# Kernel optimization log

Hardware: AMD Instinct MI355X
Metric: run time of the kernel (lower is better)

The kernel has to match this reference:

```python
import jax, jax.numpy as jnp
import numpy as np

D_MODEL = 1024
NUM_HEADS = 16
HEAD_DIM = D_MODEL // NUM_HEADS
SEQ_LEN = 4096
BATCH = 1
ROPE_THETA = 10000.0


def apply_rope(x, theta):
    # x: [B, H, S, D], interleaved pair rotation (x_{2i}, x_{2i+1})
    D = x.shape[-1]
    S = x.shape[-2]
    pos = jnp.arange(S, dtype=jnp.float32)
    inv_freq = theta ** (-jnp.arange(0, D, 2, dtype=jnp.float32) / D)  # [D/2]
    ang = pos[:, None] * inv_freq[None, :]  # [S, D/2]
    cos = jnp.cos(ang).astype(x.dtype)
    sin = jnp.sin(ang).astype(x.dtype)
    x1 = x[..., 0::2]
    x2 = x[..., 1::2]
    r1 = x1 * cos - x2 * sin
    r2 = x1 * sin + x2 * cos
    return jnp.stack([r1, r2], axis=-1).reshape(x.shape)


def setup_inputs() -> dict:
    key = jax.random.key(0)
    ks = jax.random.split(key, 5)
    s = 1.0 / np.sqrt(D_MODEL)
    return {
        "x": jax.random.normal(ks[0], (BATCH, SEQ_LEN, D_MODEL), jnp.float32),
        "Wq": jax.random.normal(ks[1], (D_MODEL, D_MODEL), jnp.float32) * s,
        "Wk": jax.random.normal(ks[2], (D_MODEL, D_MODEL), jnp.float32) * s,
        "Wv": jax.random.normal(ks[3], (D_MODEL, D_MODEL), jnp.float32) * s,
        "Wo": jax.random.normal(ks[4], (D_MODEL, D_MODEL), jnp.float32) * s,
    }


def reference(x, Wq, Wk, Wv, Wo):
    B, S, _ = x.shape
    # bias-free linear: y = x @ W.T
    def proj(W):
        y = jnp.einsum('bsd,ed->bse', x, W)
        return y.reshape(B, S, NUM_HEADS, HEAD_DIM).transpose(0, 2, 1, 3)  # [B,H,S,hd]
    q = apply_rope(proj(Wq), ROPE_THETA)
    k = apply_rope(proj(Wk), ROPE_THETA)
    v = proj(Wv)
    scale = 1.0 / jnp.sqrt(jnp.asarray(HEAD_DIM, dtype=x.dtype))
    scores = jnp.einsum('bhqd,bhkd->bhqk', q, k) * scale  # [B,H,S,S]
    causal = jnp.tril(jnp.ones((S, S), dtype=bool))
    scores = jnp.where(causal, scores, jnp.asarray(-jnp.inf, dtype=scores.dtype))
    attn = jax.nn.softmax(scores, axis=-1)
    out = jnp.einsum('bhqk,bhkd->bhqd', attn, v)
    out = out.transpose(0, 2, 1, 3).reshape(B, S, D_MODEL)
    return jnp.einsum('bsd,ed->bse', out, Wo)
```

## Files before the change

### kernel.cpp

```cpp
#include <hip/hip_runtime.h>
#include <math.h>

#define SEQ 4096
#define DM  1024
#define NH  16

typedef __attribute__((ext_vector_type(8))) short bf16x8;
typedef __attribute__((ext_vector_type(4))) float f32x4;
typedef __attribute__((ext_vector_type(16))) float f32x16;
typedef __attribute__((ext_vector_type(4))) unsigned int u32x4;

#define QSCALE 0.18033688011112042f
#define SMAX 16.0f

__device__ __forceinline__ unsigned short f2bf(float f){
  unsigned int u = __float_as_uint(f);
  u += 0x7fffu + ((u >> 16) & 1u);
  return (unsigned short)(u >> 16);
}

__device__ __forceinline__ unsigned int cvtpk(float lo, float hi){
  unsigned int r;
  asm("v_cvt_pk_bf16_f32 %0, %1, %2" : "=v"(r) : "v"(lo), "v"(hi));
  return r;
}

__device__ __forceinline__ void gload_lds16(const void* g, void* l){
  __builtin_amdgcn_global_load_lds(
      (const __attribute__((address_space(1))) unsigned int*)g,
      (__attribute__((address_space(3))) unsigned int*)l,
      16, 0, 0);
}

__global__ __launch_bounds__(256) void prep_kernel(const float* __restrict__ x,
                                                   const float* __restrict__ Wq, const float* __restrict__ Wk,
                                                   const float* __restrict__ Wv, const float* __restrict__ Wo,
                                                   unsigned short* __restrict__ xb,
                                                   unsigned short* __restrict__ wqb, unsigned short* __restrict__ wkb,
                                                   unsigned short* __restrict__ wvb, unsigned short* __restrict__ wob,
                                                   float2* __restrict__ ropetab){
  const int sel = blockIdx.y;
  if (sel < 5){
    const float* src = (sel == 0) ? x : (sel == 1) ? Wq : (sel == 2) ? Wk : (sel == 3) ? Wv : Wo;
    unsigned short* dst = (sel == 0) ? xb : (sel == 1) ? wqb : (sel == 2) ? wkb : (sel == 3) ? wvb : wob;
    const int n4 = (sel == 0) ? SEQ * DM / 4 : DM * DM / 4;
    int i = blockIdx.x * 256 + threadIdx.x;
    int stride = gridDim.x * 256;
    for (; i < n4; i += stride){
      float4 v = ((const float4*)src)[i];
      ushort4 o; o.x = f2bf(v.x); o.y = f2bf(v.y); o.z = f2bf(v.z); o.w = f2bf(v.w);
      ((ushort4*)dst)[i] = o;
    }
  } else {
    int i = blockIdx.x * 256 + threadIdx.x;
    int stride = gridDim.x * 256;
    for (; i < SEQ * 32; i += stride){
      int s = i >> 5, f = i & 31;
      double inv = exp2(-(double)f * (13.287712379549449 / 32.0));
      double a = (double)s * inv;
      const double twopi = 6.283185307179586476;
      a -= twopi * floor(a / twopi);
      float af = (float)a;
      ropetab[i] = make_float2(cosf(af), sinf(af));
    }
  }
}

__global__ __launch_bounds__(256) void qkv_gemm(const unsigned short* __restrict__ A,
                                                const unsigned short* __restrict__ Wq,
                                                const unsigned short* __restrict__ Wk,
                                                const unsigned short* __restrict__ Wv,
                                                unsigned short* __restrict__ Qo,
                                                unsigned short* __restrict__ Ko,
                                                unsigned short* __restrict__ Vto,
                                                const float2* __restrict__ rope)
{
  __shared__ unsigned short At[128 * 64];
  __shared__ unsigned short Bt[128 * 64];
  const int sel = blockIdx.x >> 3;
  const unsigned short* B = (sel == 0) ? Wq : (sel == 1) ? Wk : Wv;
  const int K = DM;
  const int t = threadIdx.x;
  const int lane = t & 63, w = t >> 6;
  const int lg = lane >> 4, lr = lane & 15;
  const int wr = w >> 1, wc = w & 1;
  const int m0 = blockIdx.y * 128, n0 = (blockIdx.x & 7) * 128;

  f32x4 acc[4][4];
  #pragma unroll
  for (int mi = 0; mi < 4; mi++)
    #pragma unroll
    for (int nj = 0; nj < 4; nj++)
      acc[mi][nj] = (f32x4){0.f, 0.f, 0.f, 0.f};

  for (int k0 = 0; k0 < K; k0 += 64){
    __syncthreads();
    #pragma unroll
    for (int r = 0; r < 4; r++){
      int idx = r * 256 + t, row = idx >> 3, ch = idx & 7, cs = ch ^ (row & 7);
      gload_lds16(&A[(size_t)(m0 + row) * K + k0 + cs * 8], &At[idx * 8]);
    }
    #pragma unroll
    for (int r = 0; r < 4; r++){
      int idx = r * 256 + t, row = idx >> 3, ch = idx & 7, cs = ch ^ (row & 7);
      gload_lds16(&B[(size_t)(n0 + row) * K + k0 + cs * 8], &Bt[idx * 8]);
    }
    __syncthreads();
    #pragma unroll
    for (int kk = 0; kk < 2; kk++){
      bf16x8 af[4], bfr[4];
      #pragma unroll
      for (int mi = 0; mi < 4; mi++){
        int row = wr * 64 + mi * 16 + lr;
        af[mi] = *(const bf16x8*)&At[row * 64 + (((kk * 4 + lg) ^ (row & 7)) << 3)];
      }
      #pragma unroll
      for (int nj = 0; nj < 4; nj++){
        int row = wc * 64 + nj * 16 + lr;
        bfr[nj] = *(const bf16x8*)&Bt[row * 64 + (((kk * 4 + lg) ^ (row & 7)) << 3)];
      }
      #pragma unroll
      for (int mi = 0; mi < 4; mi++)
        #pragma unroll
        for (int nj = 0; nj < 4; nj++)
          acc[mi][nj] = __builtin_amdgcn_mfma_f32_16x16x32_bf16(af[mi], bfr[nj], acc[mi][nj], 0, 0, 0);
    }
  }

  #pragma unroll
  for (int mi = 0; mi < 4; mi++){
    #pragma unroll
    for (int nj = 0; nj < 4; nj++){
      f32x4 v = acc[mi][nj];
      int col  = n0 + wc * 64 + nj * 16 + lr;
      int row0 = m0 + wr * 64 + mi * 16 + lg * 4;
      if (sel == 0){
        #pragma unroll
        for (int j = 0; j < 4; j++){
          float val = v[j];
          float oth = __shfl_xor(val, 1);
          int row = row0 + j;
          int i = (col & 63) >> 1;
          float2 cs = rope[row * 32 + i];
          float res = ((col & 1) == 0) ? (val * cs.x - oth * cs.y)
                                       : (oth * cs.y + val * cs.x);
          Qo[(size_t)row * DM + col] = f2bf(res * QSCALE);
        }
      } else if (sel == 1){
        const int hh = col >> 6, d = col & 63;
        #pragma unroll
        for (int j = 0; j < 4; j++){
          float val = v[j];
          float oth = __shfl_xor(val, 1);
          int row = row0 + j;
          int i = d >> 1;
          float2 cs = rope[row * 32 + i];
          float res = ((d & 1) == 0) ? (val * cs.x - oth * cs.y)
                                     : (oth * cs.y + val * cs.x);
          size_t idx = ((size_t)((hh * 128 + (row >> 5)) * 8 + (d >> 3))) * 256
                       + (row & 31) * 8 + (d & 7);
          Ko[idx] = f2bf(res);
        }
      } else {
        const int hh = col >> 6, d = col & 63;
        ushort4 pkv; pkv.x = f2bf(v[0]); pkv.y = f2bf(v[1]); pkv.z = f2bf(v[2]); pkv.w = f2bf(v[3]);
        size_t idx = ((size_t)(((hh * 2 + (d >> 5)) * 64 + (row0 >> 6)) * 8 + ((row0 >> 3) & 7))) * 256
                     + (d & 31) * 8 + (row0 & 7);
        *(ushort4*)&Vto[idx] = pkv;
      }
    }
  }
}

__global__ __launch_bounds__(256) void gemm_out(const unsigned short* __restrict__ A,
                                                const unsigned short* __restrict__ B,
                                                float* __restrict__ C)
{
  __shared__ unsigned short At[128 * 64];
  __shared__ unsigned short Bt[64 * 64];
  const int K = DM;
  const int t = threadIdx.x;
  const int lane = t & 63, w = t >> 6;
  const int lg = lane >> 4, lr = lane & 15;
  const int wr = w >> 1, wc = w & 1;
  const int m0 = blockIdx.y * 128, n0 = blockIdx.x * 64;

  f32x4 acc[4][2];
  #pragma unroll
  for (int mi = 0; mi < 4; mi++)
    #pragma unroll
    for (int nj = 0; nj < 2; nj++)
      acc[mi][nj] = (f32x4){0.f, 0.f, 0.f, 0.f};

  for (int k0 = 0; k0 < K; k0 += 64){
    __syncthreads();
    #pragma unroll
    for (int r = 0; r < 4; r++){
      int idx = r * 256 + t, row = idx >> 3, ch = idx & 7, cs = ch ^ (row & 7);
      gload_lds16(&A[(size_t)(m0 + row) * K + k0 + cs * 8], &At[idx * 8]);
    }
    #pragma unroll
    for (int r = 0; r < 2; r++){
      int idx = r * 256 + t, row = idx >> 3, ch = idx & 7, cs = ch ^ (row & 7);
      gload_lds16(&B[(size_t)(n0 + row) * K + k0 + cs * 8], &Bt[idx * 8]);
    }
    __syncthreads();
    #pragma unroll
    for (int kk = 0; kk < 2; kk++){
      bf16x8 af[4], bfr[2];
      #pragma unroll
      for (int mi = 0; mi < 4; mi++){
        int row = wr * 64 + mi * 16 + lr;
        af[mi] = *(const bf16x8*)&At[row * 64 + (((kk * 4 + lg) ^ (row & 7)) << 3)];
      }
      #pragma unroll
      for (int nj = 0; nj < 2; nj++){
        int row = wc * 32 + nj * 16 + lr;
        bfr[nj] = *(const bf16x8*)&Bt[row * 64 + (((kk * 4 + lg) ^ (row & 7)) << 3)];
      }
      #pragma unroll
      for (int mi = 0; mi < 4; mi++)
        #pragma unroll
        for (int nj = 0; nj < 2; nj++)
          acc[mi][nj] = __builtin_amdgcn_mfma_f32_16x16x32_bf16(af[mi], bfr[nj], acc[mi][nj], 0, 0, 0);
    }
  }

  #pragma unroll
  for (int mi = 0; mi < 4; mi++)
    #pragma unroll
    for (int nj = 0; nj < 2; nj++){
      f32x4 v = acc[mi][nj];
      int col  = n0 + wc * 32 + nj * 16 + lr;
      int row0 = m0 + wr * 64 + mi * 16 + lg * 4;
      #pragma unroll
      for (int j = 0; j < 4; j++)
        C[(size_t)(row0 + j) * DM + col] = v[j];
    }
}

__global__ __launch_bounds__(256, 4) void attn5_kernel(const unsigned short* __restrict__ Qb,
                                                       const unsigned short* __restrict__ Kp,
                                                       const unsigned short* __restrict__ Vp,
                                                       unsigned short* __restrict__ AO)
{
  __shared__ float oS[3][16][2][64];
  __shared__ float lS[3][32];

  const int h = blockIdx.x;
  const int qi = (int)gridDim.y - 1 - (int)blockIdx.y;
  const int q0 = qi * 32;
  const int t = threadIdx.x, w = t >> 6, lane = t & 63;
  const int ql = lane & 31, hi = lane >> 5;
  const int qrow = q0 + ql;

  const int nkt = (qi >> 1) + 1;

  bf16x8 qf[4];
  #pragma unroll
  for (int ds = 0; ds < 4; ds++)
    qf[ds] = *(const bf16x8*)&Qb[(size_t)qrow * DM + h * 64 + ds * 16 + hi * 8];

  f32x16 oacc[2];
  #pragma unroll
  for (int d = 0; d < 2; d++)
    #pragma unroll
    for (int r = 0; r < 16; r++) oacc[d][r] = 0.f;
  float lrun = 0.f;

  const bf16x8* Kf = (const bf16x8*)Kp + (size_t)h * 128 * 8 * 32;
  const bf16x8* Vf = (const bf16x8*)Vp + (size_t)h * 2 * 64 * 8 * 32;

  for (int kt = w; kt < nkt; kt += 4){
    const int k0 = kt << 6;
    const bool diag = (kt == nkt - 1);
    float p[32];

    __builtin_amdgcn_s_setprio(1);
    #pragma unroll
    for (int st = 0; st < 2; st++){
      bf16x8 kf[4];
      #pragma unroll
      for (int ds = 0; ds < 4; ds++)
        kf[ds] = Kf[(size_t)((kt * 2 + st) * 8 + ds * 2 + hi) * 32 + ql];
      f32x16 s;
      #pragma unroll
      for (int r = 0; r < 16; r++) s[r] = 0.f;
      #pragma unroll
      for (int ds = 0; ds < 4; ds++)
        s = __builtin_amdgcn_mfma_f32_32x32x16_bf16(kf[ds], qf[ds], s, 0, 0, 0);
      if (diag){
        #pragma unroll
        for (int r = 0; r < 16; r++){
          int key = k0 + st * 32 + (r & 3) + 8 * (r >> 2) + 4 * hi;
          p[st * 16 + r] = (key > qrow) ? -INFINITY : s[r];
        }
      } else {
        #pragma unroll
        for (int r = 0; r < 16; r++) p[st * 16 + r] = s[r];
      }
    }
    __builtin_amdgcn_s_setprio(0);

    float ts0 = 0.f, ts1 = 0.f, ts2 = 0.f, ts3 = 0.f;
    #pragma unroll
    for (int i = 0; i < 32; i += 4){
      p[i]     = __builtin_amdgcn_exp2f(p[i]     - SMAX); ts0 += p[i];
      p[i + 1] = __builtin_amdgcn_exp2f(p[i + 1] - SMAX); ts1 += p[i + 1];
      p[i + 2] = __builtin_amdgcn_exp2f(p[i + 2] - SMAX); ts2 += p[i + 2];
      p[i + 3] = __builtin_amdgcn_exp2f(p[i + 3] - SMAX); ts3 += p[i + 3];
    }
    float ts = (ts0 + ts1) + (ts2 + ts3);
    ts += __shfl_xor(ts, 32);
    lrun += ts;

    u32x4 pfr[4];
    #pragma unroll
    for (int ks = 0; ks < 4; ks++){
      int b = ks * 8;
      unsigned int a  = cvtpk(p[b + 0], p[b + 1]);
      unsigned int c  = cvtpk(p[b + 2], p[b + 3]);
      unsigned int bb = cvtpk(p[b + 4], p[b + 5]);
      unsigned int d  = cvtpk(p[b + 6], p[b + 7]);
      unsigned int sa = (unsigned int)__shfl_xor((int)a, 32);
      unsigned int sc = (unsigned int)__shfl_xor((int)c, 32);
      unsigned int sb = (unsigned int)__shfl_xor((int)bb, 32);
      unsigned int sd = (unsigned int)__shfl_xor((int)d, 32);
      pfr[ks][0] = hi ? sb : a;
      pfr[ks][1] = hi ? sd : c;
      pfr[ks][2] = hi ? bb : sa;
      pfr[ks][3] = hi ? d  : sc;
    }

    __builtin_amdgcn_s_setprio(1);
    #pragma unroll
    for (int dcol = 0; dcol < 2; dcol++){
      bf16x8 vf[4];
      #pragma unroll
      for (int ks = 0; ks < 4; ks++)
        vf[ks] = Vf[(size_t)((dcol * 64 + kt) * 8 + ks * 2 + hi) * 32 + ql];
      #pragma unroll
      for (int ks = 0; ks < 4; ks++){
        union { u32x4 u; bf16x8 v; } pf; pf.u = pfr[ks];
        oacc[dcol] = __builtin_amdgcn_mfma_f32_32x32x16_bf16(pf.v, vf[ks], oacc[dcol], 0, 0, 0);
      }
    }
    __builtin_amdgcn_s_setprio(0);
  }

  if (w > 0){
    if (hi == 0) lS[w - 1][ql] = lrun;
    #pragma unroll
    for (int r = 0; r < 16; r++)
      #pragma unroll
      for (int dcol = 0; dcol < 2; dcol++)
        oS[w - 1][r][hi][dcol * 32 + ql] = oacc[dcol][r];
  }
  __syncthreads();
  if (w == 0){
    float lstar = lrun + lS[0][ql] + lS[1][ql] + lS[2][ql];
    float rl = 1.f / lstar;
    #pragma unroll
    for (int r = 0; r < 16; r++){
      int rowloc = (r & 3) + 8 * (r >> 2) + 4 * hi;
      float rr = __shfl(rl, rowloc);
      int row = q0 + rowloc;
      #pragma unroll
      for (int dcol = 0; dcol < 2; dcol++){
        int dd = dcol * 32 + ql;
        float o = oacc[dcol][r] + oS[0][r][hi][dd] + oS[1][r][hi][dd] + oS[2][r][hi][dd];
        AO[(size_t)row * DM + h * 64 + dd] = f2bf(o * rr);
      }
    }
  }
}

extern "C" void kernel_launch(void* const* d_in, const int* in_sizes, int n_in,
                              void* d_out, int out_size, void* d_ws, size_t ws_size,
                              hipStream_t stream)
{
  const float* x  = (const float*)d_in[0];
  const float* Wq = (const float*)d_in[1];
  const float* Wk = (const float*)d_in[2];
  const float* Wv = (const float*)d_in[3];
  const float* Wo = (const float*)d_in[4];

  char* ws = (char*)d_ws;
  unsigned short* xb  = (unsigned short*)ws; ws += (size_t)SEQ * DM * 2;
  unsigned short* wqb = (unsigned short*)ws; ws += (size_t)DM * DM * 2;
  unsigned short* wkb = (unsigned short*)ws; ws += (size_t)DM * DM * 2;
  unsigned short* wvb = (unsigned short*)ws; ws += (size_t)DM * DM * 2;
  unsigned short* wob = (unsigned short*)ws; ws += (size_t)DM * DM * 2;
  unsigned short* Qb  = (unsigned short*)ws; ws += (size_t)SEQ * DM * 2;
  unsigned short* Kpr = (unsigned short*)ws; ws += (size_t)SEQ * DM * 2;
  unsigned short* Vpr = (unsigned short*)ws; ws += (size_t)DM * SEQ * 2;
  unsigned short* AO  = (unsigned short*)ws; ws += (size_t)SEQ * DM * 2;
  float2* ropetab     = (float2*)ws;         ws += (size_t)SEQ * 32 * sizeof(float2);

  prep_kernel<<<dim3(512, 6), 256, 0, stream>>>(x, Wq, Wk, Wv, Wo,
                                                xb, wqb, wkb, wvb, wob, ropetab);

  qkv_gemm<<<dim3(24, 32), 256, 0, stream>>>(xb, wqb, wkb, wvb, Qb, Kpr, Vpr, ropetab);

  attn5_kernel<<<dim3(NH, SEQ / 32), 256, 0, stream>>>(Qb, Kpr, Vpr, AO);

  gemm_out<<<dim3(16, 32), 256, 0, stream>>>(AO, wob, (float*)d_out);
}
```

Before: 137.5 us.

## Transpose rope table to frequency-major and pack attention partial sums as bf16

The RoPE cos/sin table is now laid out frequency-major, so each thread in the QKV epilogue fetches four consecutive rows' cos/sin with two float4 loads instead of four scattered float2 loads. Separately, the attention kernel's cross-wave reduction stores its partial output accumulators to shared memory as packed bf16 pairs instead of fp32, halving the shared buffer and its traffic. The bf16 packing of unnormalized partial sums before the final add loses precision.

```diff
diff --git a/kernel.cpp b/kernel.cpp
--- a/kernel.cpp
+++ b/kernel.cpp
@@ -55,7 +55,7 @@
     int i = blockIdx.x * 256 + threadIdx.x;
     int stride = gridDim.x * 256;
     for (; i < SEQ * 32; i += stride){
-      int s = i >> 5, f = i & 31;
+      int f = i >> 12, s = i & 4095;
       double inv = exp2(-(double)f * (13.287712379549449 / 32.0));
       double a = (double)s * inv;
       const double twopi = 6.283185307179586476;
@@ -135,28 +135,34 @@
       int col  = n0 + wc * 64 + nj * 16 + lr;
       int row0 = m0 + wr * 64 + mi * 16 + lg * 4;
       if (sel == 0){
+        int i = (col & 63) >> 1;
+        const float4* tp = (const float4*)&rope[(size_t)i * SEQ + row0];
+        float4 cA = tp[0], cB = tp[1];
+        float cj[4] = {cA.x, cA.z, cB.x, cB.z};
+        float sj[4] = {cA.y, cA.w, cB.y, cB.w};
         #pragma unroll
         for (int j = 0; j < 4; j++){
           float val = v[j];
           float oth = __shfl_xor(val, 1);
           int row = row0 + j;
-          int i = (col & 63) >> 1;
-          float2 cs = rope[row * 32 + i];
-          float res = ((col & 1) == 0) ? (val * cs.x - oth * cs.y)
-                                       : (oth * cs.y + val * cs.x);
+          float res = ((col & 1) == 0) ? (val * cj[j] - oth * sj[j])
+                                       : (oth * sj[j] + val * cj[j]);
           Qo[(size_t)row * DM + col] = f2bf(res * QSCALE);
         }
       } else if (sel == 1){
         const int hh = col >> 6, d = col & 63;
+        int i = d >> 1;
+        const float4* tp = (const float4*)&rope[(size_t)i * SEQ + row0];
+        float4 cA = tp[0], cB = tp[1];
+        float cj[4] = {cA.x, cA.z, cB.x, cB.z};
+        float sj[4] = {cA.y, cA.w, cB.y, cB.w};
         #pragma unroll
         for (int j = 0; j < 4; j++){
           float val = v[j];
           float oth = __shfl_xor(val, 1);
           int row = row0 + j;
-          int i = d >> 1;
-          float2 cs = rope[row * 32 + i];
-          float res = ((d & 1) == 0) ? (val * cs.x - oth * cs.y)
-                                     : (oth * cs.y + val * cs.x);
+          float res = ((d & 1) == 0) ? (val * cj[j] - oth * sj[j])
+                                     : (oth * sj[j] + val * cj[j]);
           size_t idx = ((size_t)((hh * 128 + (row >> 5)) * 8 + (d >> 3))) * 256
                        + (row & 31) * 8 + (d & 7);
           Ko[idx] = f2bf(res);
@@ -244,7 +250,7 @@
                                                        const unsigned short* __restrict__ Vp,
                                                        unsigned short* __restrict__ AO)
 {
-  __shared__ float oS[3][16][2][64];
+  __shared__ unsigned int oS[3][16][2][32];
   __shared__ float lS[3][32];
 
   const int h = blockIdx.x;
@@ -352,9 +358,7 @@
     if (hi == 0) lS[w - 1][ql] = lrun;
     #pragma unroll
     for (int r = 0; r < 16; r++)
-      #pragma unroll
-      for (int dcol = 0; dcol < 2; dcol++)
-        oS[w - 1][r][hi][dcol * 32 + ql] = oacc[dcol][r];
+      oS[w - 1][r][hi][ql] = cvtpk(oacc[0][r], oacc[1][r]);
   }
   __syncthreads();
   if (w == 0){
@@ -365,12 +369,15 @@
       int rowloc = (r & 3) + 8 * (r >> 2) + 4 * hi;
       float rr = __shfl(rl, rowloc);
       int row = q0 + rowloc;
-      #pragma unroll
-      for (int dcol = 0; dcol < 2; dcol++){
-        int dd = dcol * 32 + ql;
-        float o = oacc[dcol][r] + oS[0][r][hi][dd] + oS[1][r][hi][dd] + oS[2][r][hi][dd];
-        AO[(size_t)row * DM + h * 64 + dd] = f2bf(o * rr);
-      }
+      float o0 = oacc[0][r], o1 = oacc[1][r];
+      #pragma unroll
+      for (int j = 0; j < 3; j++){
+        unsigned int u = oS[j][r][hi][ql];
+        o0 += __uint_as_float(u << 16);
+        o1 += __uint_as_float(u & 0xffff0000u);
+      }
+      AO[(size_t)row * DM + h * 64 + ql]      = f2bf(o0 * rr);
+      AO[(size_t)row * DM + h * 64 + 32 + ql] = f2bf(o1 * rr);
     }
   }
 }
```

New measurement: 138.8 us. Within noise of the previous version (+0.9%).
